# Kernel optimization log

Hardware: AMD Instinct MI355X
Metric: run time of the kernel (lower is better)

Reference implementation:

```python
import jax, jax.numpy as jnp
import numpy as np

N = 50000          # nodes
E_RAND = 1_600_000 # random edges (avg degree 32)
IN = 8             # in_features
OUT = 8            # out_features
B = 16             # batch columns of x
T = 5              # edge types AFTER add_self_loops (type 1 = self loop, 2..5 = original)


def setup_inputs() -> dict:
    key = jax.random.key(0)
    k1, k2, k3, k4, k5, k6 = jax.random.split(key, 6)
    x = jax.random.normal(k1, (N * IN, B), jnp.float32)
    loops = jnp.arange(N, dtype=jnp.int32)
    # self loops prepended (type 1), random edges with types 2..T (original types shifted +1)
    src = jnp.concatenate([loops, jax.random.randint(k2, (E_RAND,), 0, N, jnp.int32)])
    dst = jnp.concatenate([loops, jax.random.randint(k3, (E_RAND,), 0, N, jnp.int32)])
    edge_types = jnp.concatenate([
        jnp.ones(N, jnp.int32),
        jax.random.randint(k4, (E_RAND,), 2, T + 1, jnp.int32),
    ])
    bound = 1.0 / np.sqrt(IN)
    # weight_vector reshaped: expand() maps ext_type = ((e-1)*OUT + i)*IN + j + 1
    W = jax.random.uniform(k5, (T, OUT, IN), jnp.float32, -bound, bound)
    # bias_vector reshaped: expand(OUT, 1) -> per (type, out-row) scalar
    Bv = jax.random.uniform(k6, (T, OUT), jnp.float32, -bound, bound)
    return dict(x=x, W=W, Bv=Bv, src=src, dst=dst, edge_types=edge_types)


def reference(x, W, Bv, src, dst, edge_types):
    T_, OUT_, IN_ = W.shape
    Nn = x.shape[0] // IN_
    xr = x.reshape(Nn, IN_, -1)                 # [N, in, B]
    Wg = W[edge_types - 1]                      # [E, out, in] per-edge weight block gather
    msg = jnp.einsum('eoi,eib->eob', Wg, xr[src])  # [E, out, B]
    y = jax.ops.segment_sum(msg, dst, num_segments=Nn)            # [N, out, B]
    yb = jax.ops.segment_sum(Bv[edge_types - 1], dst, num_segments=Nn)  # [N, out]
    y = y + yb[:, :, None]
    return y.reshape(Nn * OUT_, -1)             # [N*out, B]
```

## Files before the change

kernel.cpp:

```cpp
#include <hip/hip_runtime.h>
#include <hip/hip_fp16.h>

#define N_NODES 50000
#define E_RAND  1600000
#define IN_F    8
#define OUT_F   8
#define BATCH   16
#define T_TYPES 5

#define NB      782
#define CAP     2432
#define CHUNK   6144
#define BIN_BLOCKS  ((E_RAND + CHUNK - 1) / CHUNK)
#define CONV_BLOCKS 1563

#define OFF_BCUR   0
#define OFF_XH     4096
#define OFF_BINNED 12804096
#define WS_NEEDED  (OFF_BINNED + (size_t)NB * CAP * 4)

__global__ __launch_bounds__(512)
void zero_kernel(int* __restrict__ p, int n) {
    const int i = blockIdx.x * 512 + threadIdx.x;
    if (i < n) p[i] = 0;
}

__global__ __launch_bounds__(512)
void prep_kernel(const float* __restrict__ x, __half* __restrict__ xh,
                 const int* __restrict__ src, const int* __restrict__ dst,
                 const int* __restrict__ et,
                 int* __restrict__ bcur, int* __restrict__ binned) {
    if (blockIdx.x < CONV_BLOCKS) {
        const int b = threadIdx.x & 15;
        const int n = blockIdx.x * 32 + (threadIdx.x >> 4);
        if (n >= N_NODES) return;
        const float* xp = x + n * (IN_F * BATCH) + b;
        union { __half h[8]; uint4 u; } pk;
#pragma unroll
        for (int i = 0; i < IN_F; ++i) pk.h[i] = __float2half(xp[i * BATCH]);
        *(uint4*)(xh + (size_t)n * 128 + b * 8) = pk.u;
        return;
    }
    __shared__ int h[NB];
    __shared__ int rbase[NB];
    for (int i = threadIdx.x; i < NB; i += 512) h[i] = 0;
    __syncthreads();
    const int cbase = (blockIdx.x - CONV_BLOCKS) * CHUNK;
#pragma unroll 4
    for (int k = 0; k < CHUNK / 512; ++k) {
        const int e = cbase + k * 512 + threadIdx.x;
        if (e < E_RAND) atomicAdd(&h[dst[N_NODES + e] >> 6], 1);
    }
    __syncthreads();
    for (int i = threadIdx.x; i < NB; i += 512) {
        const int c = h[i];
        rbase[i] = c ? atomicAdd(&bcur[i], c) : 0;
        h[i] = 0;
    }
    __syncthreads();
#pragma unroll 4
    for (int k = 0; k < CHUNK / 512; ++k) {
        const int e = cbase + k * 512 + threadIdx.x;
        if (e < E_RAND) {
            const int ee  = N_NODES + e;
            const int d   = dst[ee];
            const int bkt = d >> 6;
            const int payload = ((((d & 63) << 2) | (et[ee] - 2)) << 16) | src[ee];
            binned[bkt * CAP + rbase[bkt] + atomicAdd(&h[bkt], 1)] = payload;
        }
    }
}

__device__ __forceinline__ void unpack_add(uint4 v, float* xa) {
    const __half2* hp = (const __half2*)&v;
    float2 f;
    f = __half22float2(hp[0]); xa[0] += f.x; xa[1] += f.y;
    f = __half22float2(hp[1]); xa[2] += f.x; xa[3] += f.y;
    f = __half22float2(hp[2]); xa[4] += f.x; xa[5] += f.y;
    f = __half22float2(hp[3]); xa[6] += f.x; xa[7] += f.y;
}

__global__ __launch_bounds__(512)
void sortgather_kernel(const __half* __restrict__ xh,
                       const float* __restrict__ W,
                       const float* __restrict__ Bv,
                       const int* __restrict__ bcur,
                       const int* __restrict__ binned,
                       float* __restrict__ y) {
    __shared__ int   lsort[CAP];
    __shared__ int   hist[256];
    __shared__ int   cur[256];
    __shared__ int   segoff[257];
    __shared__ float Wl[T_TYPES * OUT_F * IN_F];
    __shared__ float Bvl[T_TYPES * OUT_F];
    __shared__ int   wtot[4];

    const int bkt  = blockIdx.x;
    const int cnt  = bcur[bkt];
    const int base = bkt * CAP;
    const int t    = threadIdx.x;

    if (t < 320) Wl[t] = W[t];
    if (t >= 384 && t < 424) Bvl[t - 384] = Bv[t - 384];
    if (t < 256) hist[t] = 0;
    __syncthreads();

    for (int i = t; i < cnt; i += 512)
        atomicAdd(&hist[binned[base + i] >> 16], 1);
    __syncthreads();

    if (t < 256) {
        const int lane = t & 63;
        int inc = hist[t];
#pragma unroll
        for (int d = 1; d < 64; d <<= 1) {
            const int u = __shfl_up(inc, d);
            if (lane >= d) inc += u;
        }
        cur[t] = inc;
        if (lane == 63) wtot[t >> 6] = inc;
    }
    __syncthreads();
    if (t < 256) {
        const int wv = t >> 6;
        int wbase = 0;
        for (int w = 0; w < wv; ++w) wbase += wtot[w];
        const int excl = wbase + cur[t] - hist[t];
        segoff[t] = excl;
        cur[t]    = excl;
        if (t == 255) segoff[256] = cnt;
    }
    __syncthreads();

    for (int i = t; i < cnt; i += 512) {
        const int p = binned[base + i];
        lsort[atomicAdd(&cur[p >> 16], 1)] = p & 0xFFFF;
    }
    __syncthreads();

    const int gg   = t >> 4;
    const int b    = t & 15;
    const int boff = b * 8;
    const __half* __restrict__ xb = xh + boff;

#pragma unroll
    for (int half = 0; half < 2; ++half) {
        const int ln = gg + half * 32;
        const int n  = bkt * 64 + ln;
        if (n >= N_NODES) continue;

        float xs[IN_F];
#pragma unroll
        for (int i = 0; i < IN_F; ++i) xs[i] = 0.f;
        unpack_add(*(const uint4*)(xb + (size_t)n * 128), xs);

        float out[OUT_F];
#pragma unroll
        for (int o = 0; o < OUT_F; ++o) {
            const float4 w0 = ((const float4*)(Wl + o * IN_F))[0];
            const float4 w1 = ((const float4*)(Wl + o * IN_F))[1];
            float a = Bvl[o];
            a = fmaf(w0.x, xs[0], a); a = fmaf(w0.y, xs[1], a);
            a = fmaf(w0.z, xs[2], a); a = fmaf(w0.w, xs[3], a);
            a = fmaf(w1.x, xs[4], a); a = fmaf(w1.y, xs[5], a);
            a = fmaf(w1.z, xs[6], a); a = fmaf(w1.w, xs[7], a);
            out[o] = a;
        }

        const int* sp = segoff + ln * 4;
#pragma unroll
        for (int t4 = 0; t4 < 4; ++t4) {
            const int s0 = sp[t4];
            const int s1 = sp[t4 + 1];
            const int c  = s1 - s0;
            if (c == 0) continue;

            float xa[IN_F];
#pragma unroll
            for (int i = 0; i < IN_F; ++i) xa[i] = 0.f;

            int e = s0;
            for (; e + 4 <= s1; e += 4) {
                const int i0 = lsort[e];
                const int i1 = lsort[e + 1];
                const int i2 = lsort[e + 2];
                const int i3 = lsort[e + 3];
                const uint4 v0 = *(const uint4*)(xb + (size_t)i0 * 128);
                const uint4 v1 = *(const uint4*)(xb + (size_t)i1 * 128);
                const uint4 v2 = *(const uint4*)(xb + (size_t)i2 * 128);
                const uint4 v3 = *(const uint4*)(xb + (size_t)i3 * 128);
                unpack_add(v0, xa);
                unpack_add(v1, xa);
                unpack_add(v2, xa);
                unpack_add(v3, xa);
            }
            if (e < s1) {
                uint4 v = *(const uint4*)(xb + (size_t)lsort[e] * 128);
                for (++e; e < s1; ++e) {
                    const uint4 vn = *(const uint4*)(xb + (size_t)lsort[e] * 128);
                    unpack_add(v, xa);
                    v = vn;
                }
                unpack_add(v, xa);
            }

            const float* Wt = Wl + (t4 + 1) * (OUT_F * IN_F);
            const float* Bt = Bvl + (t4 + 1) * OUT_F;
            const float fc = (float)c;
#pragma unroll
            for (int o = 0; o < OUT_F; ++o) {
                const float4 w0 = ((const float4*)(Wt + o * IN_F))[0];
                const float4 w1 = ((const float4*)(Wt + o * IN_F))[1];
                float a = fmaf(fc, Bt[o], out[o]);
                a = fmaf(w0.x, xa[0], a); a = fmaf(w0.y, xa[1], a);
                a = fmaf(w0.z, xa[2], a); a = fmaf(w0.w, xa[3], a);
                a = fmaf(w1.x, xa[4], a); a = fmaf(w1.y, xa[5], a);
                a = fmaf(w1.z, xa[6], a); a = fmaf(w1.w, xa[7], a);
                out[o] = a;
            }
        }

        float* yp = y + (size_t)n * (OUT_F * BATCH) + b;
#pragma unroll
        for (int o = 0; o < OUT_F; ++o)
            yp[o * BATCH] = out[o];
    }
}

__global__ __launch_bounds__(256)
void selfinit_kernel(const float* __restrict__ x,
                     const float* __restrict__ W,
                     const float* __restrict__ Bv,
                     float* __restrict__ y) {
    const int b = threadIdx.x & (BATCH - 1);
    const int n = blockIdx.x * 16 + (threadIdx.x >> 4);
    if (n >= N_NODES) return;
    float xc[IN_F];
#pragma unroll
    for (int i = 0; i < IN_F; ++i) xc[i] = x[(n * IN_F + i) * BATCH + b];
#pragma unroll
    for (int o = 0; o < OUT_F; ++o) {
        float a = Bv[o];
#pragma unroll
        for (int i = 0; i < IN_F; ++i) a = fmaf(W[o * IN_F + i], xc[i], a);
        y[(n * OUT_F + o) * BATCH + b] = a;
    }
}

__global__ __launch_bounds__(256)
void direct_edge_kernel(const float* __restrict__ x,
                        const float* __restrict__ W,
                        const float* __restrict__ Bv,
                        const int* __restrict__ src,
                        const int* __restrict__ dst,
                        const int* __restrict__ et,
                        float* __restrict__ y) {
    const int tid = blockIdx.x * 256 + threadIdx.x;
    const int eg  = tid >> 4;
    const int b   = tid & (BATCH - 1);
    if (eg >= E_RAND) return;
    const int e  = N_NODES + eg;
    const int s  = src[e];
    const int d  = dst[e];
    const int ti = et[e] - 1;
    const float* __restrict__ Wt = W + ti * (OUT_F * IN_F);
    float xc[IN_F];
#pragma unroll
    for (int i = 0; i < IN_F; ++i) xc[i] = x[(s * IN_F + i) * BATCH + b];
    float* yp = y + (size_t)d * (OUT_F * BATCH) + b;
#pragma unroll
    for (int o = 0; o < OUT_F; ++o) {
        float a = Bv[ti * OUT_F + o];
#pragma unroll
        for (int i = 0; i < IN_F; ++i) a = fmaf(Wt[o * IN_F + i], xc[i], a);
        unsafeAtomicAdd(yp + o * BATCH, a);
    }
}

extern "C" void kernel_launch(void* const* d_in, const int* in_sizes, int n_in,
                              void* d_out, int out_size, void* d_ws, size_t ws_size,
                              hipStream_t stream) {
    const float* x   = (const float*)d_in[0];
    const float* W   = (const float*)d_in[1];
    const float* Bv  = (const float*)d_in[2];
    const int*   src = (const int*)d_in[3];
    const int*   dst = (const int*)d_in[4];
    const int*   et  = (const int*)d_in[5];
    float* y = (float*)d_out;

    char* ws = (char*)d_ws;
    int*    bcur   = (int*)(ws + OFF_BCUR);
    __half* xh     = (__half*)(ws + OFF_XH);
    int*    binned = (int*)(ws + OFF_BINNED);

    if (ws_size >= WS_NEEDED) {
        zero_kernel<<<2, 512, 0, stream>>>(bcur, NB);
        prep_kernel<<<CONV_BLOCKS + BIN_BLOCKS, 512, 0, stream>>>(x, xh, src, dst, et, bcur, binned);
        sortgather_kernel<<<NB, 512, 0, stream>>>(xh, W, Bv, bcur, binned, y);
    } else {
        selfinit_kernel<<<(N_NODES + 15) / 16, 256, 0, stream>>>(x, W, Bv, y);
        direct_edge_kernel<<<(E_RAND * 16 + 255) / 256, 256, 0, stream>>>(x, W, Bv, src, dst, et, y);
    }
}
```

Before: 182.6 us.

## Split each sort-gather bucket across two 256-thread blocks, reorder prep blocks

Measured after the change: 182.1 us. About the same (-0.3%).

```diff
diff --git a/kernel.cpp b/kernel.cpp
--- a/kernel.cpp
+++ b/kernel.cpp
@@ -14,6 +14,9 @@
 #define BIN_BLOCKS  ((E_RAND + CHUNK - 1) / CHUNK)
 #define CONV_BLOCKS 1563
 
+#define SG_BLOCKS (NB * 2)
+#define LCAP      1408
+
 #define OFF_BCUR   0
 #define OFF_XH     4096
 #define OFF_BINNED 12804096
@@ -30,45 +33,45 @@
                  const int* __restrict__ src, const int* __restrict__ dst,
                  const int* __restrict__ et,
                  int* __restrict__ bcur, int* __restrict__ binned) {
-    if (blockIdx.x < CONV_BLOCKS) {
-        const int b = threadIdx.x & 15;
-        const int n = blockIdx.x * 32 + (threadIdx.x >> 4);
-        if (n >= N_NODES) return;
-        const float* xp = x + n * (IN_F * BATCH) + b;
-        union { __half h[8]; uint4 u; } pk;
-#pragma unroll
-        for (int i = 0; i < IN_F; ++i) pk.h[i] = __float2half(xp[i * BATCH]);
-        *(uint4*)(xh + (size_t)n * 128 + b * 8) = pk.u;
-        return;
-    }
     __shared__ int h[NB];
     __shared__ int rbase[NB];
-    for (int i = threadIdx.x; i < NB; i += 512) h[i] = 0;
-    __syncthreads();
-    const int cbase = (blockIdx.x - CONV_BLOCKS) * CHUNK;
+    if (blockIdx.x < BIN_BLOCKS) {
+        for (int i = threadIdx.x; i < NB; i += 512) h[i] = 0;
+        __syncthreads();
+        const int cbase = blockIdx.x * CHUNK;
 #pragma unroll 4
-    for (int k = 0; k < CHUNK / 512; ++k) {
-        const int e = cbase + k * 512 + threadIdx.x;
-        if (e < E_RAND) atomicAdd(&h[dst[N_NODES + e] >> 6], 1);
-    }
-    __syncthreads();
-    for (int i = threadIdx.x; i < NB; i += 512) {
-        const int c = h[i];
-        rbase[i] = c ? atomicAdd(&bcur[i], c) : 0;
-        h[i] = 0;
-    }
-    __syncthreads();
+        for (int k = 0; k < CHUNK / 512; ++k) {
+            const int e = cbase + k * 512 + threadIdx.x;
+            if (e < E_RAND) atomicAdd(&h[dst[N_NODES + e] >> 6], 1);
+        }
+        __syncthreads();
+        for (int i = threadIdx.x; i < NB; i += 512) {
+            const int c = h[i];
+            rbase[i] = c ? atomicAdd(&bcur[i], c) : 0;
+            h[i] = 0;
+        }
+        __syncthreads();
 #pragma unroll 4
-    for (int k = 0; k < CHUNK / 512; ++k) {
-        const int e = cbase + k * 512 + threadIdx.x;
-        if (e < E_RAND) {
-            const int ee  = N_NODES + e;
-            const int d   = dst[ee];
-            const int bkt = d >> 6;
-            const int payload = ((((d & 63) << 2) | (et[ee] - 2)) << 16) | src[ee];
-            binned[bkt * CAP + rbase[bkt] + atomicAdd(&h[bkt], 1)] = payload;
-        }
-    }
+        for (int k = 0; k < CHUNK / 512; ++k) {
+            const int e = cbase + k * 512 + threadIdx.x;
+            if (e < E_RAND) {
+                const int ee  = N_NODES + e;
+                const int d   = dst[ee];
+                const int bkt = d >> 6;
+                const int payload = ((((d & 63) << 2) | (et[ee] - 2)) << 16) | src[ee];
+                binned[bkt * CAP + rbase[bkt] + atomicAdd(&h[bkt], 1)] = payload;
+            }
+        }
+        return;
+    }
+    const int b = threadIdx.x & 15;
+    const int n = (blockIdx.x - BIN_BLOCKS) * 32 + (threadIdx.x >> 4);
+    if (n >= N_NODES) return;
+    const float* xp = x + n * (IN_F * BATCH) + b;
+    union { __half hh[8]; uint4 u; } pk;
+#pragma unroll
+    for (int i = 0; i < IN_F; ++i) pk.hh[i] = __float2half(xp[i * BATCH]);
+    *(uint4*)(xh + (size_t)n * 128 + b * 8) = pk.u;
 }
 
 __device__ __forceinline__ void unpack_add(uint4 v, float* xa) {
@@ -80,36 +83,39 @@
     f = __half22float2(hp[3]); xa[6] += f.x; xa[7] += f.y;
 }
 
-__global__ __launch_bounds__(512)
+__global__ __launch_bounds__(256)
 void sortgather_kernel(const __half* __restrict__ xh,
                        const float* __restrict__ W,
                        const float* __restrict__ Bv,
                        const int* __restrict__ bcur,
                        const int* __restrict__ binned,
                        float* __restrict__ y) {
-    __shared__ int   lsort[CAP];
-    __shared__ int   hist[256];
-    __shared__ int   cur[256];
-    __shared__ int   segoff[257];
+    __shared__ int   lsort[LCAP];
+    __shared__ int   hist[128];
+    __shared__ int   cur[128];
+    __shared__ int   segoff[129];
     __shared__ float Wl[T_TYPES * OUT_F * IN_F];
     __shared__ float Bvl[T_TYPES * OUT_F];
-    __shared__ int   wtot[4];
-
-    const int bkt  = blockIdx.x;
+    __shared__ int   wtot[2];
+
+    const int bkt  = blockIdx.x >> 1;
+    const int hf   = blockIdx.x & 1;
     const int cnt  = bcur[bkt];
     const int base = bkt * CAP;
     const int t    = threadIdx.x;
 
-    if (t < 320) Wl[t] = W[t];
-    if (t >= 384 && t < 424) Bvl[t - 384] = Bv[t - 384];
-    if (t < 256) hist[t] = 0;
-    __syncthreads();
-
-    for (int i = t; i < cnt; i += 512)
-        atomicAdd(&hist[binned[base + i] >> 16], 1);
-    __syncthreads();
-
-    if (t < 256) {
+    for (int i = t; i < 320; i += 256) Wl[i] = W[i];
+    if (t >= 192 && t < 232) Bvl[t - 192] = Bv[t - 192];
+    if (t < 128) hist[t] = 0;
+    __syncthreads();
+
+    for (int i = t; i < cnt; i += 256) {
+        const int k = binned[base + i] >> 16;
+        if ((k >> 7) == hf) atomicAdd(&hist[k & 127], 1);
+    }
+    __syncthreads();
+
+    if (t < 128) {
         const int lane = t & 63;
         int inc = hist[t];
 #pragma unroll
@@ -121,20 +127,20 @@
         if (lane == 63) wtot[t >> 6] = inc;
     }
     __syncthreads();
-    if (t < 256) {
-        const int wv = t >> 6;
-        int wbase = 0;
-        for (int w = 0; w < wv; ++w) wbase += wtot[w];
-        const int excl = wbase + cur[t] - hist[t];
+    if (t < 128) {
+        const int wbase = (t >= 64) ? wtot[0] : 0;
+        const int excl  = wbase + cur[t] - hist[t];
         segoff[t] = excl;
         cur[t]    = excl;
-        if (t == 255) segoff[256] = cnt;
-    }
-    __syncthreads();
-
-    for (int i = t; i < cnt; i += 512) {
+        if (t == 127) segoff[128] = wtot[0] + wtot[1];
+    }
+    __syncthreads();
+
+    for (int i = t; i < cnt; i += 256) {
         const int p = binned[base + i];
-        lsort[atomicAdd(&cur[p >> 16], 1)] = p & 0xFFFF;
+        const int k = p >> 16;
+        if ((k >> 7) == hf)
+            lsort[atomicAdd(&cur[k & 127], 1)] = p & 0xFFFF;
     }
     __syncthreads();
 
@@ -145,8 +151,8 @@
 
 #pragma unroll
     for (int half = 0; half < 2; ++half) {
-        const int ln = gg + half * 32;
-        const int n  = bkt * 64 + ln;
+        const int ln = gg + half * 16;
+        const int n  = bkt * 64 + hf * 32 + ln;
         if (n >= N_NODES) continue;
 
         float xs[IN_F];
@@ -295,8 +301,8 @@
 
     if (ws_size >= WS_NEEDED) {
         zero_kernel<<<2, 512, 0, stream>>>(bcur, NB);
-        prep_kernel<<<CONV_BLOCKS + BIN_BLOCKS, 512, 0, stream>>>(x, xh, src, dst, et, bcur, binned);
-        sortgather_kernel<<<NB, 512, 0, stream>>>(xh, W, Bv, bcur, binned, y);
+        prep_kernel<<<BIN_BLOCKS + CONV_BLOCKS, 512, 0, stream>>>(x, xh, src, dst, et, bcur, binned);
+        sortgather_kernel<<<SG_BLOCKS, 256, 0, stream>>>(xh, W, Bv, bcur, binned, y);
     } else {
         selfinit_kernel<<<(N_NODES + 15) / 16, 256, 0, stream>>>(x, W, Bv, y);
         direct_edge_kernel<<<(E_RAND * 16 + 255) / 256, 256, 0, stream>>>(x, W, Bv, src, dst, et, y);
```
